# Kernel optimization log

Measured on AMD Instinct MI355X. Metric: run time of the kernel, lower is better.

The kernel has to match this reference:

```python
import jax, jax.numpy as jnp
import numpy as np

NUM_EMBEDDINGS = 512
EMBEDDING_DIM = 64
COMMITMENT_COST = 0.25


def setup_inputs() -> dict:
    key = jax.random.key(0)
    k1, k2 = jax.random.split(key)
    inputs = jax.random.normal(k1, (128, 1024, EMBEDDING_DIM), dtype=jnp.float32)
    embedding = jax.random.normal(k2, (NUM_EMBEDDINGS, EMBEDDING_DIM), dtype=jnp.float32)
    return {"inputs": inputs, "embedding": embedding}


def reference(inputs, embedding):
    """Eval-mode forward of VectorQuantizerEMA.

    Returns (loss, quantized, perplexity, encodings), matching the torch module
    with self.training == False.
    """
    input_shape = inputs.shape
    flat = inputs.reshape(-1, EMBEDDING_DIM)                      # [N, D]
    distances = (
        jnp.sum(flat ** 2, axis=1, keepdims=True)
        + jnp.sum(embedding ** 2, axis=1)
        - 2.0 * flat @ embedding.T
    )
    encoding_indices = jnp.argmin(distances, axis=1)              # [N]
    encodings = jax.nn.one_hot(encoding_indices, NUM_EMBEDDINGS, dtype=jnp.float32)  # [N, K]
    # quantized = onehot @ W  ==  gather rows (same math, cheaper)
    quantized = jnp.take(embedding, encoding_indices, axis=0).reshape(input_shape)

    e_latent_loss = jnp.mean((jax.lax.stop_gradient(quantized) - inputs) ** 2)
    loss = COMMITMENT_COST * e_latent_loss

    # straight-through estimator
    quantized = inputs + jax.lax.stop_gradient(quantized - inputs)

    avg_probs = jnp.mean(encodings, axis=0)                       # [K]
    perplexity = jnp.exp(-jnp.sum(avg_probs * jnp.log(avg_probs + 1e-10)))
    return loss, quantized, perplexity, encodings
```

## Files before the change

### kernel.cpp

```cpp
#include <hip/hip_runtime.h>
#include <math.h>


#define NK 512
#define ND 64
#define NROWS 131072
#define ROWS_PB 64
#define BLOCK 256
#define NBLOCKS (NROWS / ROWS_PB)
#define NTILES 32
#define XSTRIDE 68
#define MARGIN 0.02f

#define Q_OFF    1
#define PERP_OFF 8388609
#define ENC_OFF  8388610

typedef float vf2 __attribute__((ext_vector_type(2)));
typedef float vf4 __attribute__((ext_vector_type(4)));
typedef short vs8 __attribute__((ext_vector_type(8)));

__device__ __forceinline__ unsigned short bf16_rne(float v) {
    union { float f; unsigned int u; } a; a.f = v;
    return (unsigned short)((a.u + 0x7FFFu + ((a.u >> 16) & 1u)) >> 16);
}
__device__ __forceinline__ float bf16_to_f(unsigned short s) {
    union { unsigned int u; float f; } a; a.u = ((unsigned int)s) << 16;
    return a.f;
}

__global__ __launch_bounds__(64) void vq_prep(const float* __restrict__ emb,
                                              float* __restrict__ eknorm,
                                              unsigned int* __restrict__ efrag) {
    const int t = blockIdx.x;
    const int l = threadIdx.x;
    const int c = t * 16 + (l & 15);
    const int quad = l >> 4;
    #pragma unroll
    for (int f = 0; f < 4; ++f) {
        const int kbase = (f & 1) * 32 + quad * 8;
        unsigned int w[4];
        #pragma unroll
        for (int d = 0; d < 4; ++d) {
            float v0 = emb[c * ND + kbase + 2 * d];
            float v1 = emb[c * ND + kbase + 2 * d + 1];
            unsigned short h0 = bf16_rne(v0), h1 = bf16_rne(v1);
            unsigned short l0 = bf16_rne(v0 - bf16_to_f(h0));
            unsigned short l1 = bf16_rne(v1 - bf16_to_f(h1));
            unsigned short e0 = (f < 2) ? h0 : l0;
            unsigned short e1 = (f < 2) ? h1 : l1;
            w[d] = (unsigned int)e0 | ((unsigned int)e1 << 16);
        }
        unsigned int* dst = efrag + ((size_t)(t * 4 + f) * 64 + l) * 4;
        dst[0] = w[0]; dst[1] = w[1]; dst[2] = w[2]; dst[3] = w[3];
    }
    if (quad == 0) {
        const vf4* er = (const vf4*)(emb + c * ND);
        float s0 = 0.f, s1 = 0.f, s2 = 0.f, s3 = 0.f;
        #pragma unroll
        for (int j = 0; j < 16; ++j) {
            vf4 v = er[j];
            s0 += v.x * v.x; s1 += v.y * v.y; s2 += v.z * v.z; s3 += v.w * v.w;
        }
        eknorm[c] = (s0 + s1) + (s2 + s3);
    }
}

__global__ __launch_bounds__(BLOCK) void vq_main(const float* __restrict__ x,
                                                 const float* __restrict__ emb,
                                                 const float* __restrict__ eknorm,
                                                 const unsigned int* __restrict__ efrag,
                                                 float* __restrict__ out,
                                                 int* __restrict__ g_counts,
                                                 float* __restrict__ g_loss) {
    __shared__ float lds_x[ROWS_PB * XSTRIDE];
    __shared__ float ek_lds[NK];
    __shared__ float d1s[ROWS_PB], d2s[ROWS_PB];
    __shared__ int   i1s[ROWS_PB], i2s[ROWS_PB];
    __shared__ int   idx_s[ROWS_PB];
    __shared__ float red[4];

    const int tid  = threadIdx.x;
    const int wave = tid >> 6;
    const int lane = tid & 63;
    const int col  = lane & 15;
    const int quad = lane >> 4;

    {
        const vf4* xp = (const vf4*)(x + (size_t)blockIdx.x * ROWS_PB * ND);
        #pragma unroll
        for (int i = 0; i < 4; ++i) {
            int e4 = tid + i * BLOCK;
            int r  = e4 >> 4;
            int c4 = (e4 & 15) * 4;
            *(vf4*)&lds_x[r * XSTRIDE + c4] = xp[e4];
        }
        ek_lds[tid] = eknorm[tid];
        ek_lds[tid + 256] = eknorm[tid + 256];
    }
    __syncthreads();

    const int arow = wave * 16 + col;
    vs8 ah0, ah1, al0, al1;
    {
        const float* xr = &lds_x[arow * XSTRIDE];
        #pragma unroll
        for (int j = 0; j < 8; ++j) {
            float va = xr[quad * 8 + j];
            float vb = xr[32 + quad * 8 + j];
            unsigned short ha = bf16_rne(va);
            unsigned short hb = bf16_rne(vb);
            ah0[j] = (short)ha; al0[j] = (short)bf16_rne(va - bf16_to_f(ha));
            ah1[j] = (short)hb; al1[j] = (short)bf16_rne(vb - bf16_to_f(hb));
        }
    }

    float d1[4], d2[4];
    int   i1[4], i2[4];
    #pragma unroll
    for (int r = 0; r < 4; ++r) { d1[r] = INFINITY; d2[r] = INFINITY; i1[r] = 0x7FFFFFFF; i2[r] = 0x7FFFFFFF; }

    const vs8* bbase = (const vs8*)efrag;
    vs8 b0 = bbase[(0 * 4 + 0) * 64 + lane];
    vs8 b1 = bbase[(0 * 4 + 1) * 64 + lane];
    vs8 b2 = bbase[(0 * 4 + 2) * 64 + lane];
    vs8 b3 = bbase[(0 * 4 + 3) * 64 + lane];

    for (int t = 0; t < NTILES; ++t) {
        vs8 n0, n1, n2, n3;
        if (t + 1 < NTILES) {
            n0 = bbase[((t + 1) * 4 + 0) * 64 + lane];
            n1 = bbase[((t + 1) * 4 + 1) * 64 + lane];
            n2 = bbase[((t + 1) * 4 + 2) * 64 + lane];
            n3 = bbase[((t + 1) * 4 + 3) * 64 + lane];
        }
        vf4 acc = {0.f, 0.f, 0.f, 0.f};
        acc = __builtin_amdgcn_mfma_f32_16x16x32_bf16(ah0, b0, acc, 0, 0, 0);
        acc = __builtin_amdgcn_mfma_f32_16x16x32_bf16(ah1, b1, acc, 0, 0, 0);
        acc = __builtin_amdgcn_mfma_f32_16x16x32_bf16(al0, b0, acc, 0, 0, 0);
        acc = __builtin_amdgcn_mfma_f32_16x16x32_bf16(al1, b1, acc, 0, 0, 0);
        acc = __builtin_amdgcn_mfma_f32_16x16x32_bf16(ah0, b2, acc, 0, 0, 0);
        acc = __builtin_amdgcn_mfma_f32_16x16x32_bf16(ah1, b3, acc, 0, 0, 0);
        acc = __builtin_amdgcn_mfma_f32_16x16x32_bf16(al0, b2, acc, 0, 0, 0);
        acc = __builtin_amdgcn_mfma_f32_16x16x32_bf16(al1, b3, acc, 0, 0, 0);

        const float ek = ek_lds[t * 16 + col];
        const int cidx = t * 16 + col;
        #pragma unroll
        for (int r = 0; r < 4; ++r) {
            float d = ek - 2.f * acc[r];
            bool lt1 = d < d1[r];
            bool lt2 = d < d2[r];
            float nd2 = lt1 ? d1[r] : (lt2 ? d : d2[r]);
            int   ni2 = lt1 ? i1[r] : (lt2 ? cidx : i2[r]);
            d2[r] = nd2; i2[r] = ni2;
            d1[r] = lt1 ? d : d1[r];
            i1[r] = lt1 ? cidx : i1[r];
        }
        b0 = n0; b1 = n1; b2 = n2; b3 = n3;
    }

    #pragma unroll
    for (int m = 8; m >= 1; m >>= 1) {
        #pragma unroll
        for (int r = 0; r < 4; ++r) {
            float od1 = __shfl_xor(d1[r], m);
            int   oi1 = __shfl_xor(i1[r], m);
            float od2 = __shfl_xor(d2[r], m);
            int   oi2 = __shfl_xor(i2[r], m);
            bool aF = (d1[r] < od1) || (d1[r] == od1 && i1[r] < oi1);
            float n1 = aF ? d1[r] : od1;  int ni1 = aF ? i1[r] : oi1;
            float ca = aF ? od1 : d1[r];  int cia = aF ? oi1 : i1[r];
            float cb = aF ? d2[r] : od2;  int cib = aF ? i2[r] : oi2;
            bool bF = (cb < ca) || (cb == ca && cib < cia);
            float n2 = bF ? cb : ca;      int ni2 = bF ? cib : cia;
            d1[r] = n1; i1[r] = ni1; d2[r] = n2; i2[r] = ni2;
        }
    }
    if (col == 0) {
        #pragma unroll
        for (int r = 0; r < 4; ++r) {
            int lr = wave * 16 + quad * 4 + r;
            d1s[lr] = d1[r]; i1s[lr] = i1[r];
            d2s[lr] = d2[r]; i2s[lr] = i2[r];
        }
    }
    __syncthreads();

    if (tid < ROWS_PB) {
        int am = i1s[tid];
        if (d2s[tid] - d1s[tid] < MARGIN) {
            int ia = i1s[tid], ib = i2s[tid];
            const float* xr = &lds_x[tid * XSTRIDE];
            float da, db;
            {
                const vf4* er = (const vf4*)(emb + ia * ND);
                float s0 = 0.f, s1 = 0.f, s2 = 0.f, s3 = 0.f;
                #pragma unroll
                for (int j = 0; j < 16; ++j) {
                    vf4 v = er[j];
                    s0 += xr[4 * j] * v.x; s1 += xr[4 * j + 1] * v.y;
                    s2 += xr[4 * j + 2] * v.z; s3 += xr[4 * j + 3] * v.w;
                }
                da = ek_lds[ia] - 2.f * ((s0 + s1) + (s2 + s3));
            }
            {
                const vf4* er = (const vf4*)(emb + ib * ND);
                float s0 = 0.f, s1 = 0.f, s2 = 0.f, s3 = 0.f;
                #pragma unroll
                for (int j = 0; j < 16; ++j) {
                    vf4 v = er[j];
                    s0 += xr[4 * j] * v.x; s1 += xr[4 * j + 1] * v.y;
                    s2 += xr[4 * j + 2] * v.z; s3 += xr[4 * j + 3] * v.w;
                }
                db = ek_lds[ib] - 2.f * ((s0 + s1) + (s2 + s3));
            }
            am = ((db < da) || (db == da && ib < ia)) ? ib : ia;
        }
        idx_s[tid] = am;
        atomicAdd(&g_counts[am], 1);
    }
    __syncthreads();

    float lacc = 0.f;
    {
        float* qout = out + Q_OFF + (size_t)blockIdx.x * ROWS_PB * ND;
        #pragma unroll 4
        for (int i = 0; i < 16; ++i) {
            int p = tid + i * BLOCK;
            int r = p >> 6;
            int c = p & 63;
            float q = emb[idx_s[r] * ND + c];
            float xv = lds_x[r * XSTRIDE + c];
            qout[p] = q;
            float dlt = q - xv;
            lacc += dlt * dlt;
        }
    }
    #pragma unroll
    for (int off = 32; off >= 1; off >>= 1) lacc += __shfl_down(lacc, off);
    if (lane == 0) red[wave] = lacc;
    __syncthreads();
    if (tid == 0) atomicAdd(g_loss, (red[0] + red[1]) + (red[2] + red[3]));

    {
        vf2* eout = (vf2*)(out + ENC_OFF) + (size_t)blockIdx.x * ROWS_PB * NK / 2;
        #pragma unroll 4
        for (int i = 0; i < 64; ++i) {
            int p = tid + i * BLOCK;
            int r = p >> 8;
            int c2 = p & 255;
            int am = idx_s[r];
            vf2 v = {0.f, 0.f};
            if ((am >> 1) == c2) {
                if (am & 1) v.y = 1.f; else v.x = 1.f;
            }
            __builtin_nontemporal_store(v, &eout[p]);
        }
    }
}

__global__ __launch_bounds__(512) void vq_final(const int* __restrict__ g_counts,
                                                const float* __restrict__ g_loss,
                                                float* __restrict__ out) {
    __shared__ float red[8];
    int t = threadIdx.x;
    float p = (float)g_counts[t] * (1.0f / (float)NROWS);
    float h = p * logf(p + 1e-10f);
    #pragma unroll
    for (int off = 32; off >= 1; off >>= 1) h += __shfl_down(h, off);
    if ((t & 63) == 0) red[t >> 6] = h;
    __syncthreads();
    if (t == 0) {
        float s = 0.f;
        #pragma unroll
        for (int i = 0; i < 8; ++i) s += red[i];
        out[PERP_OFF] = expf(-s);
        out[0] = 0.25f * g_loss[0] / (float)(NROWS * ND);
    }
}

extern "C" void kernel_launch(void* const* d_in, const int* in_sizes, int n_in,
                              void* d_out, int out_size, void* d_ws, size_t ws_size,
                              hipStream_t stream) {
    const float* x   = (const float*)d_in[0];
    const float* emb = (const float*)d_in[1];
    float* out = (float*)d_out;

    int*          g_counts = (int*)d_ws;
    float*        g_loss   = (float*)((char*)d_ws + 2048);
    float*        eknorm   = (float*)((char*)d_ws + 4096);
    unsigned int* efrag    = (unsigned int*)((char*)d_ws + 8192);

    (void)hipMemsetAsync(d_ws, 0, 4096, stream);

    vq_prep<<<NTILES, 64, 0, stream>>>(emb, eknorm, efrag);
    vq_main<<<NBLOCKS, BLOCK, 0, stream>>>(x, emb, eknorm, efrag, out, g_counts, g_loss);
    vq_final<<<1, 512, 0, stream>>>(g_counts, g_loss, out);
}
```

Measured before the change: 378.7 us.

## Double rows per block, fold final reduction into last block, drop memset

Each block now handles 128 rows, and each wave computes two 16-row MFMA tiles that share every loaded embedding fragment. This halves the per-row fragment traffic and gives independent MFMA chains room to interleave. The separate final kernel is replaced by a last-block-done atomic counter, and the workspace memset moves into the prep kernel, cutting two launches. The cost is higher register pressure and half as many blocks to spread across the device.

```diff
diff --git a/kernel.cpp b/kernel.cpp
--- a/kernel.cpp
+++ b/kernel.cpp
@@ -5,7 +5,7 @@
 #define NK 512
 #define ND 64
 #define NROWS 131072
-#define ROWS_PB 64
+#define ROWS_PB 128
 #define BLOCK 256
 #define NBLOCKS (NROWS / ROWS_PB)
 #define NTILES 32
@@ -31,9 +31,14 @@
 
 __global__ __launch_bounds__(64) void vq_prep(const float* __restrict__ emb,
                                               float* __restrict__ eknorm,
-                                              unsigned int* __restrict__ efrag) {
+                                              unsigned int* __restrict__ efrag,
+                                              int* __restrict__ ws_zero) {
     const int t = blockIdx.x;
     const int l = threadIdx.x;
+    if (t == 0) {
+        #pragma unroll
+        for (int i = 0; i < 16; ++i) ws_zero[l + i * 64] = 0;
+    }
     const int c = t * 16 + (l & 15);
     const int quad = l >> 4;
     #pragma unroll
@@ -66,19 +71,21 @@
     }
 }
 
-__global__ __launch_bounds__(BLOCK) void vq_main(const float* __restrict__ x,
-                                                 const float* __restrict__ emb,
-                                                 const float* __restrict__ eknorm,
-                                                 const unsigned int* __restrict__ efrag,
-                                                 float* __restrict__ out,
-                                                 int* __restrict__ g_counts,
-                                                 float* __restrict__ g_loss) {
+__global__ __launch_bounds__(BLOCK, 4) void vq_main(const float* __restrict__ x,
+                                                    const float* __restrict__ emb,
+                                                    const float* __restrict__ eknorm,
+                                                    const unsigned int* __restrict__ efrag,
+                                                    float* __restrict__ out,
+                                                    int* __restrict__ g_counts,
+                                                    float* __restrict__ g_loss,
+                                                    unsigned int* __restrict__ g_done) {
     __shared__ float lds_x[ROWS_PB * XSTRIDE];
     __shared__ float ek_lds[NK];
     __shared__ float d1s[ROWS_PB], d2s[ROWS_PB];
     __shared__ int   i1s[ROWS_PB], i2s[ROWS_PB];
     __shared__ int   idx_s[ROWS_PB];
     __shared__ float red[4];
+    __shared__ int   amLast;
 
     const int tid  = threadIdx.x;
     const int wave = tid >> 6;
@@ -89,7 +96,7 @@
     {
         const vf4* xp = (const vf4*)(x + (size_t)blockIdx.x * ROWS_PB * ND);
         #pragma unroll
-        for (int i = 0; i < 4; ++i) {
+        for (int i = 0; i < 8; ++i) {
             int e4 = tid + i * BLOCK;
             int r  = e4 >> 4;
             int c4 = (e4 & 15) * 4;
@@ -100,31 +107,42 @@
     }
     __syncthreads();
 
-    const int arow = wave * 16 + col;
-    vs8 ah0, ah1, al0, al1;
+    const int rowA = wave * 32 + col;
+    const int rowB = rowA + 16;
+    vs8 ah0a, ah1a, al0a, al1a, ah0b, ah1b, al0b, al1b;
     {
-        const float* xr = &lds_x[arow * XSTRIDE];
+        const float* xr = &lds_x[rowA * XSTRIDE];
         #pragma unroll
         for (int j = 0; j < 8; ++j) {
             float va = xr[quad * 8 + j];
             float vb = xr[32 + quad * 8 + j];
             unsigned short ha = bf16_rne(va);
             unsigned short hb = bf16_rne(vb);
-            ah0[j] = (short)ha; al0[j] = (short)bf16_rne(va - bf16_to_f(ha));
-            ah1[j] = (short)hb; al1[j] = (short)bf16_rne(vb - bf16_to_f(hb));
-        }
-    }
-
-    float d1[4], d2[4];
-    int   i1[4], i2[4];
+            ah0a[j] = (short)ha; al0a[j] = (short)bf16_rne(va - bf16_to_f(ha));
+            ah1a[j] = (short)hb; al1a[j] = (short)bf16_rne(vb - bf16_to_f(hb));
+        }
+        const float* xs = &lds_x[rowB * XSTRIDE];
+        #pragma unroll
+        for (int j = 0; j < 8; ++j) {
+            float va = xs[quad * 8 + j];
+            float vb = xs[32 + quad * 8 + j];
+            unsigned short ha = bf16_rne(va);
+            unsigned short hb = bf16_rne(vb);
+            ah0b[j] = (short)ha; al0b[j] = (short)bf16_rne(va - bf16_to_f(ha));
+            ah1b[j] = (short)hb; al1b[j] = (short)bf16_rne(vb - bf16_to_f(hb));
+        }
+    }
+
+    float d1[8], d2[8];
+    int   i1[8], i2[8];
     #pragma unroll
-    for (int r = 0; r < 4; ++r) { d1[r] = INFINITY; d2[r] = INFINITY; i1[r] = 0x7FFFFFFF; i2[r] = 0x7FFFFFFF; }
+    for (int s = 0; s < 8; ++s) { d1[s] = INFINITY; d2[s] = INFINITY; i1[s] = 0x7FFFFFFF; i2[s] = 0x7FFFFFFF; }
 
     const vs8* bbase = (const vs8*)efrag;
-    vs8 b0 = bbase[(0 * 4 + 0) * 64 + lane];
-    vs8 b1 = bbase[(0 * 4 + 1) * 64 + lane];
-    vs8 b2 = bbase[(0 * 4 + 2) * 64 + lane];
-    vs8 b3 = bbase[(0 * 4 + 3) * 64 + lane];
+    vs8 b0 = bbase[0 * 64 + lane];
+    vs8 b1 = bbase[1 * 64 + lane];
+    vs8 b2 = bbase[2 * 64 + lane];
+    vs8 b3 = bbase[3 * 64 + lane];
 
     for (int t = 0; t < NTILES; ++t) {
         vs8 n0, n1, n2, n3;
@@ -134,28 +152,48 @@
             n2 = bbase[((t + 1) * 4 + 2) * 64 + lane];
             n3 = bbase[((t + 1) * 4 + 3) * 64 + lane];
         }
-        vf4 acc = {0.f, 0.f, 0.f, 0.f};
-        acc = __builtin_amdgcn_mfma_f32_16x16x32_bf16(ah0, b0, acc, 0, 0, 0);
-        acc = __builtin_amdgcn_mfma_f32_16x16x32_bf16(ah1, b1, acc, 0, 0, 0);
-        acc = __builtin_amdgcn_mfma_f32_16x16x32_bf16(al0, b0, acc, 0, 0, 0);
-        acc = __builtin_amdgcn_mfma_f32_16x16x32_bf16(al1, b1, acc, 0, 0, 0);
-        acc = __builtin_amdgcn_mfma_f32_16x16x32_bf16(ah0, b2, acc, 0, 0, 0);
-        acc = __builtin_amdgcn_mfma_f32_16x16x32_bf16(ah1, b3, acc, 0, 0, 0);
-        acc = __builtin_amdgcn_mfma_f32_16x16x32_bf16(al0, b2, acc, 0, 0, 0);
-        acc = __builtin_amdgcn_mfma_f32_16x16x32_bf16(al1, b3, acc, 0, 0, 0);
+        vf4 accA = {0.f, 0.f, 0.f, 0.f};
+        vf4 accB = {0.f, 0.f, 0.f, 0.f};
+        accA = __builtin_amdgcn_mfma_f32_16x16x32_bf16(ah0a, b0, accA, 0, 0, 0);
+        accB = __builtin_amdgcn_mfma_f32_16x16x32_bf16(ah0b, b0, accB, 0, 0, 0);
+        accA = __builtin_amdgcn_mfma_f32_16x16x32_bf16(ah1a, b1, accA, 0, 0, 0);
+        accB = __builtin_amdgcn_mfma_f32_16x16x32_bf16(ah1b, b1, accB, 0, 0, 0);
+        accA = __builtin_amdgcn_mfma_f32_16x16x32_bf16(al0a, b0, accA, 0, 0, 0);
+        accB = __builtin_amdgcn_mfma_f32_16x16x32_bf16(al0b, b0, accB, 0, 0, 0);
+        accA = __builtin_amdgcn_mfma_f32_16x16x32_bf16(al1a, b1, accA, 0, 0, 0);
+        accB = __builtin_amdgcn_mfma_f32_16x16x32_bf16(al1b, b1, accB, 0, 0, 0);
+        accA = __builtin_amdgcn_mfma_f32_16x16x32_bf16(ah0a, b2, accA, 0, 0, 0);
+        accB = __builtin_amdgcn_mfma_f32_16x16x32_bf16(ah0b, b2, accB, 0, 0, 0);
+        accA = __builtin_amdgcn_mfma_f32_16x16x32_bf16(ah1a, b3, accA, 0, 0, 0);
+        accB = __builtin_amdgcn_mfma_f32_16x16x32_bf16(ah1b, b3, accB, 0, 0, 0);
+        accA = __builtin_amdgcn_mfma_f32_16x16x32_bf16(al0a, b2, accA, 0, 0, 0);
+        accB = __builtin_amdgcn_mfma_f32_16x16x32_bf16(al0b, b2, accB, 0, 0, 0);
+        accA = __builtin_amdgcn_mfma_f32_16x16x32_bf16(al1a, b3, accA, 0, 0, 0);
+        accB = __builtin_amdgcn_mfma_f32_16x16x32_bf16(al1b, b3, accB, 0, 0, 0);
 
         const float ek = ek_lds[t * 16 + col];
         const int cidx = t * 16 + col;
         #pragma unroll
         for (int r = 0; r < 4; ++r) {
-            float d = ek - 2.f * acc[r];
-            bool lt1 = d < d1[r];
-            bool lt2 = d < d2[r];
-            float nd2 = lt1 ? d1[r] : (lt2 ? d : d2[r]);
-            int   ni2 = lt1 ? i1[r] : (lt2 ? cidx : i2[r]);
-            d2[r] = nd2; i2[r] = ni2;
-            d1[r] = lt1 ? d : d1[r];
-            i1[r] = lt1 ? cidx : i1[r];
+            {
+                float d = ek - 2.f * accA[r];
+                bool lt1 = d < d1[r];
+                bool lt2 = d < d2[r];
+                d2[r] = lt1 ? d1[r] : (lt2 ? d : d2[r]);
+                i2[r] = lt1 ? i1[r] : (lt2 ? cidx : i2[r]);
+                d1[r] = lt1 ? d : d1[r];
+                i1[r] = lt1 ? cidx : i1[r];
+            }
+            {
+                const int s = r + 4;
+                float d = ek - 2.f * accB[r];
+                bool lt1 = d < d1[s];
+                bool lt2 = d < d2[s];
+                d2[s] = lt1 ? d1[s] : (lt2 ? d : d2[s]);
+                i2[s] = lt1 ? i1[s] : (lt2 ? cidx : i2[s]);
+                d1[s] = lt1 ? d : d1[s];
+                i1[s] = lt1 ? cidx : i1[s];
+            }
         }
         b0 = n0; b1 = n1; b2 = n2; b3 = n3;
     }
@@ -163,26 +201,26 @@
     #pragma unroll
     for (int m = 8; m >= 1; m >>= 1) {
         #pragma unroll
-        for (int r = 0; r < 4; ++r) {
-            float od1 = __shfl_xor(d1[r], m);
-            int   oi1 = __shfl_xor(i1[r], m);
-            float od2 = __shfl_xor(d2[r], m);
-            int   oi2 = __shfl_xor(i2[r], m);
-            bool aF = (d1[r] < od1) || (d1[r] == od1 && i1[r] < oi1);
-            float n1 = aF ? d1[r] : od1;  int ni1 = aF ? i1[r] : oi1;
-            float ca = aF ? od1 : d1[r];  int cia = aF ? oi1 : i1[r];
-            float cb = aF ? d2[r] : od2;  int cib = aF ? i2[r] : oi2;
+        for (int s = 0; s < 8; ++s) {
+            float od1 = __shfl_xor(d1[s], m);
+            int   oi1 = __shfl_xor(i1[s], m);
+            float od2 = __shfl_xor(d2[s], m);
+            int   oi2 = __shfl_xor(i2[s], m);
+            bool aF = (d1[s] < od1) || (d1[s] == od1 && i1[s] < oi1);
+            float n1 = aF ? d1[s] : od1;  int ni1 = aF ? i1[s] : oi1;
+            float ca = aF ? od1 : d1[s];  int cia = aF ? oi1 : i1[s];
+            float cb = aF ? d2[s] : od2;  int cib = aF ? i2[s] : oi2;
             bool bF = (cb < ca) || (cb == ca && cib < cia);
             float n2 = bF ? cb : ca;      int ni2 = bF ? cib : cia;
-            d1[r] = n1; i1[r] = ni1; d2[r] = n2; i2[r] = ni2;
+            d1[s] = n1; i1[s] = ni1; d2[s] = n2; i2[s] = ni2;
         }
     }
     if (col == 0) {
         #pragma unroll
-        for (int r = 0; r < 4; ++r) {
-            int lr = wave * 16 + quad * 4 + r;
-            d1s[lr] = d1[r]; i1s[lr] = i1[r];
-            d2s[lr] = d2[r]; i2s[lr] = i2[r];
+        for (int s = 0; s < 8; ++s) {
+            int lr = wave * 32 + (s >> 2) * 16 + quad * 4 + (s & 3);
+            d1s[lr] = d1[s]; i1s[lr] = i1[s];
+            d2s[lr] = d2[s]; i2s[lr] = i2[s];
         }
     }
     __syncthreads();
@@ -226,7 +264,7 @@
     {
         float* qout = out + Q_OFF + (size_t)blockIdx.x * ROWS_PB * ND;
         #pragma unroll 4
-        for (int i = 0; i < 16; ++i) {
+        for (int i = 0; i < 32; ++i) {
             int p = tid + i * BLOCK;
             int r = p >> 6;
             int c = p & 63;
@@ -246,7 +284,7 @@
     {
         vf2* eout = (vf2*)(out + ENC_OFF) + (size_t)blockIdx.x * ROWS_PB * NK / 2;
         #pragma unroll 4
-        for (int i = 0; i < 64; ++i) {
+        for (int i = 0; i < 128; ++i) {
             int p = tid + i * BLOCK;
             int r = p >> 8;
             int c2 = p & 255;
@@ -258,25 +296,35 @@
             __builtin_nontemporal_store(v, &eout[p]);
         }
     }
-}
-
-__global__ __launch_bounds__(512) void vq_final(const int* __restrict__ g_counts,
-                                                const float* __restrict__ g_loss,
-                                                float* __restrict__ out) {
-    __shared__ float red[8];
-    int t = threadIdx.x;
-    float p = (float)g_counts[t] * (1.0f / (float)NROWS);
-    float h = p * logf(p + 1e-10f);
-    #pragma unroll
-    for (int off = 32; off >= 1; off >>= 1) h += __shfl_down(h, off);
-    if ((t & 63) == 0) red[t >> 6] = h;
-    __syncthreads();
-    if (t == 0) {
-        float s = 0.f;
-        #pragma unroll
-        for (int i = 0; i < 8; ++i) s += red[i];
-        out[PERP_OFF] = expf(-s);
-        out[0] = 0.25f * g_loss[0] / (float)(NROWS * ND);
+
+    if (tid == 0) {
+        __threadfence();
+        unsigned int prev = __hip_atomic_fetch_add(g_done, 1u, __ATOMIC_ACQ_REL,
+                                                   __HIP_MEMORY_SCOPE_AGENT);
+        amLast = (prev == (unsigned int)(NBLOCKS - 1)) ? 1 : 0;
+    }
+    __syncthreads();
+    if (amLast) {
+        float h = 0.f;
+        #pragma unroll
+        for (int i = 0; i < 2; ++i) {
+            int t = tid + i * 256;
+            int cnt = __hip_atomic_load(&g_counts[t], __ATOMIC_RELAXED,
+                                        __HIP_MEMORY_SCOPE_AGENT);
+            float p = (float)cnt * (1.0f / (float)NROWS);
+            h += p * logf(p + 1e-10f);
+        }
+        #pragma unroll
+        for (int off = 32; off >= 1; off >>= 1) h += __shfl_down(h, off);
+        if (lane == 0) red[wave] = h;
+        __syncthreads();
+        if (tid == 0) {
+            float s = (red[0] + red[1]) + (red[2] + red[3]);
+            out[PERP_OFF] = expf(-s);
+            float ls = __hip_atomic_load(g_loss, __ATOMIC_RELAXED,
+                                         __HIP_MEMORY_SCOPE_AGENT);
+            out[0] = 0.25f * ls / (float)(NROWS * ND);
+        }
     }
 }
 
@@ -289,12 +337,11 @@
 
     int*          g_counts = (int*)d_ws;
     float*        g_loss   = (float*)((char*)d_ws + 2048);
+    unsigned int* g_done   = (unsigned int*)((char*)d_ws + 2056);
     float*        eknorm   = (float*)((char*)d_ws + 4096);
     unsigned int* efrag    = (unsigned int*)((char*)d_ws + 8192);
 
-    (void)hipMemsetAsync(d_ws, 0, 4096, stream);
-
-    vq_prep<<<NTILES, 64, 0, stream>>>(emb, eknorm, efrag);
-    vq_main<<<NBLOCKS, BLOCK, 0, stream>>>(x, emb, eknorm, efrag, out, g_counts, g_loss);
-    vq_final<<<1, 512, 0, stream>>>(g_counts, g_loss, out);
-}
+    vq_prep<<<NTILES, 64, 0, stream>>>(emb, eknorm, efrag, (int*)d_ws);
+    vq_main<<<NBLOCKS, BLOCK, 0, stream>>>(x, emb, eknorm, efrag, out,
+                                           g_counts, g_loss, g_done);
+}
```

After: 519.3 us. 1.37x slower.

## Split VQ main kernel into distance and store kernels, fold finalization in

Applied to the files above, without the earlier changes.

Splits the fused kernel into two. A distance/argmin kernel writes 16-bit indices to workspace. A separate store kernel then writes the quantized rows, the loss and the one-hot encodings, rereading x from global memory. The memset and the final kernel are removed: vq_prep zeroes the workspace, and the last store block, found through an atomic done counter, computes perplexity and loss. This trades an extra pass over x and an extra launch for lighter kernels that may overlap better. Quantized output now uses nontemporal stores.

```diff
diff --git a/kernel.cpp b/kernel.cpp
--- a/kernel.cpp
+++ b/kernel.cpp
@@ -31,9 +31,14 @@
 
 __global__ __launch_bounds__(64) void vq_prep(const float* __restrict__ emb,
                                               float* __restrict__ eknorm,
-                                              unsigned int* __restrict__ efrag) {
+                                              unsigned int* __restrict__ efrag,
+                                              int* __restrict__ ws_zero) {
     const int t = blockIdx.x;
     const int l = threadIdx.x;
+    if (t == 0) {
+        #pragma unroll
+        for (int i = 0; i < 16; ++i) ws_zero[l + i * 64] = 0;
+    }
     const int c = t * 16 + (l & 15);
     const int quad = l >> 4;
     #pragma unroll
@@ -66,19 +71,16 @@
     }
 }
 
-__global__ __launch_bounds__(BLOCK) void vq_main(const float* __restrict__ x,
+__global__ __launch_bounds__(BLOCK) void vq_dist(const float* __restrict__ x,
                                                  const float* __restrict__ emb,
                                                  const float* __restrict__ eknorm,
                                                  const unsigned int* __restrict__ efrag,
-                                                 float* __restrict__ out,
-                                                 int* __restrict__ g_counts,
-                                                 float* __restrict__ g_loss) {
+                                                 unsigned short* __restrict__ g_idx,
+                                                 int* __restrict__ g_counts) {
     __shared__ float lds_x[ROWS_PB * XSTRIDE];
     __shared__ float ek_lds[NK];
     __shared__ float d1s[ROWS_PB], d2s[ROWS_PB];
     __shared__ int   i1s[ROWS_PB], i2s[ROWS_PB];
-    __shared__ int   idx_s[ROWS_PB];
-    __shared__ float red[4];
 
     const int tid  = threadIdx.x;
     const int wave = tid >> 6;
@@ -217,22 +219,41 @@
             }
             am = ((db < da) || (db == da && ib < ia)) ? ib : ia;
         }
-        idx_s[tid] = am;
+        g_idx[blockIdx.x * ROWS_PB + tid] = (unsigned short)am;
         atomicAdd(&g_counts[am], 1);
     }
+}
+
+__global__ __launch_bounds__(BLOCK) void vq_store(const float* __restrict__ x,
+                                                  const float* __restrict__ emb,
+                                                  const unsigned short* __restrict__ g_idx,
+                                                  const int* __restrict__ g_counts,
+                                                  float* __restrict__ g_loss,
+                                                  unsigned int* __restrict__ g_done,
+                                                  float* __restrict__ out) {
+    __shared__ int   idx_l[ROWS_PB];
+    __shared__ float red[4];
+    __shared__ int   amLast;
+
+    const int tid  = threadIdx.x;
+    const int wave = tid >> 6;
+    const int lane = tid & 63;
+
+    if (tid < ROWS_PB) idx_l[tid] = g_idx[blockIdx.x * ROWS_PB + tid];
     __syncthreads();
 
     float lacc = 0.f;
     {
+        const float* xin = x + (size_t)blockIdx.x * ROWS_PB * ND;
         float* qout = out + Q_OFF + (size_t)blockIdx.x * ROWS_PB * ND;
         #pragma unroll 4
         for (int i = 0; i < 16; ++i) {
             int p = tid + i * BLOCK;
             int r = p >> 6;
             int c = p & 63;
-            float q = emb[idx_s[r] * ND + c];
-            float xv = lds_x[r * XSTRIDE + c];
-            qout[p] = q;
+            float q = emb[idx_l[r] * ND + c];
+            float xv = xin[p];
+            __builtin_nontemporal_store(q, &qout[p]);
             float dlt = q - xv;
             lacc += dlt * dlt;
         }
@@ -250,7 +271,7 @@
             int p = tid + i * BLOCK;
             int r = p >> 8;
             int c2 = p & 255;
-            int am = idx_s[r];
+            int am = idx_l[r];
             vf2 v = {0.f, 0.f};
             if ((am >> 1) == c2) {
                 if (am & 1) v.y = 1.f; else v.x = 1.f;
@@ -258,25 +279,35 @@
             __builtin_nontemporal_store(v, &eout[p]);
         }
     }
-}
-
-__global__ __launch_bounds__(512) void vq_final(const int* __restrict__ g_counts,
-                                                const float* __restrict__ g_loss,
-                                                float* __restrict__ out) {
-    __shared__ float red[8];
-    int t = threadIdx.x;
-    float p = (float)g_counts[t] * (1.0f / (float)NROWS);
-    float h = p * logf(p + 1e-10f);
-    #pragma unroll
-    for (int off = 32; off >= 1; off >>= 1) h += __shfl_down(h, off);
-    if ((t & 63) == 0) red[t >> 6] = h;
-    __syncthreads();
-    if (t == 0) {
-        float s = 0.f;
-        #pragma unroll
-        for (int i = 0; i < 8; ++i) s += red[i];
-        out[PERP_OFF] = expf(-s);
-        out[0] = 0.25f * g_loss[0] / (float)(NROWS * ND);
+
+    if (tid == 0) {
+        __threadfence();
+        unsigned int prev = __hip_atomic_fetch_add(g_done, 1u, __ATOMIC_ACQ_REL,
+                                                   __HIP_MEMORY_SCOPE_AGENT);
+        amLast = (prev == (unsigned int)(NBLOCKS - 1)) ? 1 : 0;
+    }
+    __syncthreads();
+    if (amLast) {
+        float h = 0.f;
+        #pragma unroll
+        for (int i = 0; i < 2; ++i) {
+            int t = tid + i * 256;
+            int cnt = __hip_atomic_load(&g_counts[t], __ATOMIC_RELAXED,
+                                        __HIP_MEMORY_SCOPE_AGENT);
+            float p = (float)cnt * (1.0f / (float)NROWS);
+            h += p * logf(p + 1e-10f);
+        }
+        #pragma unroll
+        for (int off = 32; off >= 1; off >>= 1) h += __shfl_down(h, off);
+        if (lane == 0) red[wave] = h;
+        __syncthreads();
+        if (tid == 0) {
+            float s = (red[0] + red[1]) + (red[2] + red[3]);
+            out[PERP_OFF] = expf(-s);
+            float ls = __hip_atomic_load(g_loss, __ATOMIC_RELAXED,
+                                         __HIP_MEMORY_SCOPE_AGENT);
+            out[0] = 0.25f * ls / (float)(NROWS * ND);
+        }
     }
 }
 
@@ -287,14 +318,14 @@
     const float* emb = (const float*)d_in[1];
     float* out = (float*)d_out;
 
-    int*          g_counts = (int*)d_ws;
-    float*        g_loss   = (float*)((char*)d_ws + 2048);
-    float*        eknorm   = (float*)((char*)d_ws + 4096);
-    unsigned int* efrag    = (unsigned int*)((char*)d_ws + 8192);
-
-    (void)hipMemsetAsync(d_ws, 0, 4096, stream);
-
-    vq_prep<<<NTILES, 64, 0, stream>>>(emb, eknorm, efrag);
-    vq_main<<<NBLOCKS, BLOCK, 0, stream>>>(x, emb, eknorm, efrag, out, g_counts, g_loss);
-    vq_final<<<1, 512, 0, stream>>>(g_counts, g_loss, out);
-}
+    int*            g_counts = (int*)d_ws;
+    float*          g_loss   = (float*)((char*)d_ws + 2048);
+    unsigned int*   g_done   = (unsigned int*)((char*)d_ws + 2056);
+    float*          eknorm   = (float*)((char*)d_ws + 4096);
+    unsigned int*   efrag    = (unsigned int*)((char*)d_ws + 8192);
+    unsigned short* g_idx    = (unsigned short*)((char*)d_ws + 139264);
+
+    vq_prep<<<NTILES, 64, 0, stream>>>(emb, eknorm, efrag, (int*)d_ws);
+    vq_dist<<<NBLOCKS, BLOCK, 0, stream>>>(x, emb, eknorm, efrag, g_idx, g_counts);
+    vq_store<<<NBLOCKS, BLOCK, 0, stream>>>(x, emb, g_idx, g_counts, g_loss, g_done, out);
+}
```

New measurement: 641.4 us. 69.4% more time.
